# Optimization experiments

Hardware: AMD Instinct MI355X
Metric: run time of the kernel (lower is better)

Reference implementation:

```python
import jax, jax.numpy as jnp
import numpy as np

BN_EPS = 1e-5

def _bn(x, gamma, beta, relu=True):
    # training-mode BatchNorm over all dims except channel (last)
    axes = tuple(range(x.ndim - 1))
    mu = jnp.mean(x, axes, keepdims=True)
    var = jnp.var(x, axes, keepdims=True)
    y = (x - mu) / jnp.sqrt(var + BN_EPS) * gamma + beta
    return jax.nn.relu(y) if relu else y

def _l2norm(x, eps):
    # F.normalize: x / max(||x||, eps)
    n = jnp.sqrt(jnp.sum(x * x, axis=-1, keepdims=True))
    return x / jnp.maximum(n, eps)

def setup_inputs() -> dict:
    key = jax.random.key(0)
    ks = jax.random.split(key, 16)
    B, N, H, W, C = 2, 512, 16, 32, 64
    IN_DIM = 10 + C + C + 2  # 140
    MLP3 = [128, 64]
    s = 0.02
    inp = {
        "warped_xyz": jax.random.normal(ks[0], (B, N, 3), jnp.float32),
        "warped_points": jax.random.normal(ks[1], (B, N, C), jnp.float32),
        "RF3": jax.random.normal(ks[2], (B, C, H, W), jnp.float32),
        "RF3_index": jax.random.normal(ks[3], (B, 3, H, W), jnp.float32),
        "lidar_z": jax.random.uniform(ks[4], (B, N, 1), jnp.float32),
        # conv1x1 stack (mlp3)
        "W1": jax.random.normal(ks[5], (IN_DIM, MLP3[0]), jnp.float32) * s,
        "b1": jnp.zeros((MLP3[0],), jnp.float32),
        "g1": jnp.ones((MLP3[0],), jnp.float32),
        "be1": jnp.zeros((MLP3[0],), jnp.float32),
        "W2": jax.random.normal(ks[6], (MLP3[0], MLP3[1]), jnp.float32) * s,
        "b2": jnp.zeros((MLP3[1],), jnp.float32),
        "g2": jnp.ones((MLP3[1],), jnp.float32),
        "be2": jnp.zeros((MLP3[1],), jnp.float32),
        # conv1d stack (mlp4 = [feats_dim//2], then 2 logits)
        "M1w": jax.random.normal(ks[7], (MLP3[1], MLP3[1] // 2), jnp.float32) * s,
        "M1b": jnp.zeros((MLP3[1] // 2,), jnp.float32),
        "M1g": jnp.ones((MLP3[1] // 2,), jnp.float32),
        "M1be": jnp.zeros((MLP3[1] // 2,), jnp.float32),
        "M2w": jax.random.normal(ks[8], (MLP3[1] // 2, 2), jnp.float32) * s,
        "M2b": jnp.zeros((2,), jnp.float32),
    }
    return inp

def reference(warped_xyz, warped_points, RF3, RF3_index, lidar_z,
              W1, b1, g1, be1, W2, b2, g2, be2,
              M1w, M1b, M1g, M1be, M2w, M2b):
    B, N, _ = warped_xyz.shape
    _, Ci, H, W_ = RF3.shape
    M = H * W_
    RF3_bnc = RF3.transpose(0, 2, 3, 1).reshape(B, M, Ci)          # [B,M,C]
    idx_bnc = RF3_index.transpose(0, 2, 3, 1).reshape(B, M, 3)     # [B,M,3]

    src_xyz = warped_xyz[:, :, None, :]                             # [B,N,1,3]
    dst_xyz = idx_bnc[:, None, :, :]                                # [B,1,M,3]
    euc = (src_xyz - dst_xyz)[..., :2]                              # [B,N,M,2]
    euc_norm = jnp.sqrt(euc[..., 0:1] ** 2 + euc[..., 1:2] ** 2)    # [B,N,M,1]

    xyz_z = (warped_xyz * lidar_z)[:, :, None, :]                   # [B,N,1,3]
    src_pts = warped_points[:, :, None, :]                          # [B,N,1,C]
    dst_pts = RF3_bnc[:, None, :, :]                                # [B,1,M,C]

    geom = jnp.concatenate([
        jnp.broadcast_to(xyz_z, (B, N, M, 3)),
        jnp.broadcast_to(src_pts[..., :2], (B, N, M, 2)),
        jnp.broadcast_to(dst_xyz[..., :2], (B, N, M, 2)),
        euc, euc_norm], axis=-1)                                    # [B,N,M,10]
    desc = jnp.concatenate([
        jnp.broadcast_to(src_pts, (B, N, M, Ci)),
        jnp.broadcast_to(dst_pts, (B, N, M, Ci))], axis=-1)         # [B,N,M,2C]

    # cal_sim: cosine sim between lidar feats (src) and image feats (dst)
    src_n = _l2norm(warped_points, 1e-12)
    dst_n = _l2norm(RF3_bnc, 1e-12)
    cos = jnp.einsum('bnc,bmc->bnm', src_n, dst_n)                  # [B,N,M]
    s1 = cos / (jnp.max(cos, axis=2, keepdims=True) + 1e-6)         # src->dst norm
    s2 = cos / (jnp.max(cos, axis=1, keepdims=True) + 1e-10)        # dst->src norm
    sim = jnp.stack([s1, s2], axis=-1)                              # [B,N,M,2]

    feats = jnp.concatenate([geom, desc, sim], axis=-1)             # [B,N,M,140]
    feats = _bn(jnp.einsum('bnmi,io->bnmo', feats, W1) + b1, g1, be1)
    feats = _bn(jnp.einsum('bnmi,io->bnmo', feats, W2) + b2, g2, be2)

    aw = jax.nn.softmax(jnp.max(feats, axis=-1), axis=-1)           # [B,N,M]
    att = jnp.einsum('bnm,bnmc->bnc', aw, feats)                    # [B,N,C]

    att = _bn(att @ M1w + M1b, M1g, M1be)
    logits = att @ M2w + M2b                                        # [B,N,2]
    return logits
```

## Files before the change

### kernel.cpp

```cpp
#include <hip/hip_runtime.h>
#include <hip/hip_bf16.h>

#define B_ 2
#define N_ 512
#define M_ 512
#define C_ 64
#define O1 128
#define O2 64
#define O3 32
#define PBIG 524288.0f
#define P3   1024.0f

typedef short s8v __attribute__((ext_vector_type(8)));
typedef float f4v __attribute__((ext_vector_type(4)));

#define WS_SRCN 0
#define WS_DSTN 65536
#define WS_P0   0
#define WS_U    131072
#define WS_Z    131072
#define WS_V    262144
#define WS_DXY  393216
#define WS_COS  395264
#define WS_RMAX 919552
#define WS_ROWS 920576
#define WS_COLS 923648
#define WS_A1C  926720
#define WS_SC2P 935936
#define WS_ST2  936960
#define WS_ST3  945152
#define WS_CMAX 949248
#define WS_W2F  950272
#define WS_W9S  954368
#define WS_X2   961536

__device__ __forceinline__ unsigned short f2bf(float f){
  unsigned u = __float_as_uint(f);
  unsigned r = (u + 0x7fffu + ((u >> 16) & 1u)) >> 16;
  return (unsigned short)r;
}
__device__ __forceinline__ float bf2f(unsigned short h){
  return __uint_as_float(((unsigned)h) << 16);
}
__device__ __forceinline__ unsigned pk2(float lo, float hi){
  return (unsigned)f2bf(lo) | ((unsigned)f2bf(hi) << 16);
}
__device__ __forceinline__ unsigned pk_trunc(float lo, float hi){
  return __builtin_amdgcn_perm(__float_as_uint(hi), __float_as_uint(lo), 0x07060302u);
}
__device__ __forceinline__ f4v relu4(f4v z){
  z[0] = fmaxf(z[0], 0.f); z[1] = fmaxf(z[1], 0.f);
  z[2] = fmaxf(z[2], 0.f); z[3] = fmaxf(z[3], 0.f);
  return z;
}

__global__ __launch_bounds__(128) void k1(const float* __restrict__ wxyz,
    const float* __restrict__ wpts, const float* __restrict__ lz,
    const float* __restrict__ rf3, const float* __restrict__ rf3i,
    const float* __restrict__ W1, float* __restrict__ ws){
  int t = threadIdx.x;
  if (blockIdx.x < 1024){
    int blk = blockIdx.x; int b = blk >> 9, n = blk & 511;
    int bn = b*N_ + n;
    __shared__ float wp[64]; __shared__ float sxyz[3]; __shared__ float slz; __shared__ float srn;
    if (t < 64) wp[t] = wpts[bn*64 + t];
    if (t >= 64 && t < 67) sxyz[t-64] = wxyz[bn*3 + (t-64)];
    if (t == 67) slz = lz[bn];
    __syncthreads();
    if (t < 64){
      float v = wp[t]*wp[t];
      v += __shfl_down(v,32); v += __shfl_down(v,16); v += __shfl_down(v,8);
      v += __shfl_down(v,4);  v += __shfl_down(v,2);  v += __shfl_down(v,1);
      if (t == 0) srn = 1.0f / fmaxf(sqrtf(v), 1e-12f);
    }
    __syncthreads();
    if (t < 64) ws[WS_SRCN + bn*64 + t] = wp[t]*srn;
    int o = t;
    float x = sxyz[0], y = sxyz[1], z = sxyz[2], l = slz;
    float acc = x*l*W1[0*O1+o] + y*l*W1[1*O1+o] + z*l*W1[2*O1+o]
              + wp[0]*W1[3*O1+o] + wp[1]*W1[4*O1+o]
              + x*W1[7*O1+o] + y*W1[8*O1+o];
    #pragma unroll 8
    for (int c = 0; c < 64; ++c) acc += wp[c]*W1[(10+c)*O1+o];
    ws[WS_U + bn*O1 + o] = acc;
  } else {
    int blk = blockIdx.x - 1024; int b = blk >> 9, m = blk & 511;
    int bm = b*M_ + m;
    __shared__ float rf[64]; __shared__ float sdx, sdy, srn2;
    if (t < 64) rf[t] = rf3[(b*64 + t)*512 + m];
    if (t == 64) sdx = rf3i[(b*3 + 0)*512 + m];
    if (t == 65) sdy = rf3i[(b*3 + 1)*512 + m];
    __syncthreads();
    if (t < 64){
      float v = rf[t]*rf[t];
      v += __shfl_down(v,32); v += __shfl_down(v,16); v += __shfl_down(v,8);
      v += __shfl_down(v,4);  v += __shfl_down(v,2);  v += __shfl_down(v,1);
      if (t == 0) srn2 = 1.0f / fmaxf(sqrtf(v), 1e-12f);
    }
    __syncthreads();
    if (t < 64) ws[WS_DSTN + bm*64 + t] = rf[t]*srn2;
    if (t == 0){ ws[WS_DXY + bm*2+0] = sdx; ws[WS_DXY + bm*2+1] = sdy; }
    int o = t;
    float acc = sdx*(W1[5*O1+o] - W1[7*O1+o]) + sdy*(W1[6*O1+o] - W1[8*O1+o]);
    #pragma unroll 8
    for (int c = 0; c < 64; ++c) acc += rf[c]*W1[(74+c)*O1+o];
    ws[WS_V + bm*O1 + o] = acc;
  }
}

__global__ __launch_bounds__(256) void k2(float* __restrict__ ws){
  int blk = blockIdx.x; int b = blk >> 9, n = blk & 511; int t = threadIdx.x;
  int bn = b*N_ + n;
  __shared__ __align__(16) float sn[64];
  __shared__ float dnt[64*65];
  __shared__ float part[4*64];
  if (t < 64) sn[t] = ws[WS_SRCN + bn*64 + t];
  float lmax = -3.4e38f;
  for (int chunk = 0; chunk < 8; ++chunk){
    __syncthreads();
    const float4* src = (const float4*)(ws + WS_DSTN + (size_t)(b*M_ + chunk*64)*64);
    #pragma unroll
    for (int i = 0; i < 4; ++i){
      float4 v = src[t + i*256];
      int base = (t + i*256)*4; int mm = base >> 6, c = base & 63;
      float* dp = &dnt[mm*65 + c];
      dp[0]=v.x; dp[1]=v.y; dp[2]=v.z; dp[3]=v.w;
    }
    __syncthreads();
    {
      int mm = t & 63, cg = t >> 6;
      const float* dr = &dnt[mm*65 + cg*16];
      const float* sr = &sn[cg*16];
      float p = 0.f;
      #pragma unroll
      for (int k = 0; k < 16; ++k) p += sr[k]*dr[k];
      part[cg*64 + mm] = p;
    }
    __syncthreads();
    if (t < 64){
      float d = part[t] + part[64+t] + part[128+t] + part[192+t];
      ws[WS_COS + bn*M_ + chunk*64 + t] = d;
      lmax = fmaxf(lmax, d);
    }
  }
  if (t < 64){
    lmax = fmaxf(lmax, __shfl_xor(lmax,32)); lmax = fmaxf(lmax, __shfl_xor(lmax,16));
    lmax = fmaxf(lmax, __shfl_xor(lmax,8));  lmax = fmaxf(lmax, __shfl_xor(lmax,4));
    lmax = fmaxf(lmax, __shfl_xor(lmax,2));  lmax = fmaxf(lmax, __shfl_xor(lmax,1));
    if (t == 0) ws[WS_RMAX + bn] = 1.0f / (lmax + 1e-6f);
  }
}

__global__ __launch_bounds__(256) void k2r(const float* __restrict__ wxyz, float* __restrict__ ws){
  int blk = blockIdx.x;
  int b = blk >> 5; int c0 = (blk & 31)*16;
  int t = threadIdx.x;
  int cl = t & 15, seg = t >> 4;
  int col = c0 + cl;
  int bm = b*M_ + col;
  float dx = ws[WS_DXY + bm*2+0], dy = ws[WS_DXY + bm*2+1];
  float mx = -3.4e38f, se = 0.f, sc = 0.f, s1c = 0.f;
  for (int i = 0; i < 32; ++i){
    int bn = b*N_ + seg*32 + i;
    float cv = ws[WS_COS + (size_t)bn*M_ + col];
    float ri = ws[WS_RMAX + bn];
    float sx = wxyz[bn*3+0], sy = wxyz[bn*3+1];
    float ex = sx-dx, ey = sy-dy;
    se += sqrtf(ex*ex + ey*ey);
    mx = fmaxf(mx, cv);
    sc += cv;
    s1c += cv*ri;
  }
  __shared__ float r0[256], r1[256], r2[256], r3[256];
  r0[t]=mx; r1[t]=se; r2[t]=s1c; r3[t]=sc;
  __syncthreads();
  for (int s = 8; s > 0; s >>= 1){
    if (seg < s){
      int o2 = t + s*16;
      r0[t] = fmaxf(r0[t], r0[o2]); r1[t] += r1[o2]; r2[t] += r2[o2]; r3[t] += r3[o2];
    }
    __syncthreads();
  }
  if (t < 16){
    int bmw = b*M_ + c0 + t;
    float ci = 1.0f/(r0[t] + 1e-10f);
    ws[WS_CMAX + bmw] = ci;
    ws[WS_COLS + bmw] = r1[t];
    ws[WS_COLS + 1024 + bmw] = r2[t];
    ws[WS_COLS + 2048 + bmw] = r3[t]*ci;
  }
}

__global__ __launch_bounds__(256) void k3a(const float* __restrict__ wxyz, float* __restrict__ ws){
  int bn = blockIdx.x; int b = bn >> 9; int t = threadIdx.x;
  float ri = ws[WS_RMAX + bn];
  float sx = wxyz[bn*3+0], sy = wxyz[bn*3+1];
  float q[9];
  #pragma unroll
  for (int j = 0; j < 9; ++j) q[j] = 0.f;
  #pragma unroll
  for (int k = 0; k < 2; ++k){
    int m = t + k*256;
    float2 d = *(const float2*)(ws + WS_DXY + (size_t)(b*M_+m)*2);
    float ex = sx-d.x, ey = sy-d.y;
    float en = sqrtf(ex*ex + ey*ey);
    float cv = ws[WS_COS + (size_t)bn*M_ + m];
    float ci = ws[WS_CMAX + b*M_ + m];
    float s2 = cv*ci;
    q[0]+=en; q[1]+=cv; q[2]+=s2; q[3]+=en*en; q[4]+=cv*cv; q[5]+=s2*s2;
    q[6]+=en*cv; q[7]+=en*s2; q[8]+=cv*cv*ci;
  }
  #pragma unroll
  for (int j = 0; j < 9; ++j){
    float v = q[j];
    v += __shfl_xor(v,1); v += __shfl_xor(v,2); v += __shfl_xor(v,4);
    v += __shfl_xor(v,8); v += __shfl_xor(v,16); v += __shfl_xor(v,32);
    q[j] = v;
  }
  __shared__ float wr[9][4];
  int w = t >> 6;
  if ((t & 63) == 0){
    #pragma unroll
    for (int j = 0; j < 9; ++j) wr[j][w] = q[j];
  }
  __syncthreads();
  if (t < 9){
    float Q = wr[t][0] + wr[t][1] + wr[t][2] + wr[t][3];
    float f = (t==1 || t==6 || t==8) ? ri : ((t==4) ? ri*ri : 1.0f);
    float s = f*Q;
    if (t < 3) ws[WS_ROWS + t*1024 + bn] = s;
    atomicAdd(&ws[WS_SC2P + (bn & 63)*16 + t], s);
  }
}

__global__ __launch_bounds__(256) void k3s(const float* __restrict__ W1,
    const float* __restrict__ b1, const float* __restrict__ g1,
    const float* __restrict__ be1, float* __restrict__ ws){
  int o = blockIdx.x; int t = threadIdx.x;
  __shared__ float scal[9];
  __shared__ float wr[12][4];
  if (t < 9){
    float s = 0.f;
    #pragma unroll 8
    for (int r = 0; r < 64; ++r) s += ws[WS_SC2P + r*16 + t];
    scal[t] = s;
  }
  float b1o = b1[o];
  float a[12];
  #pragma unroll
  for (int j = 0; j < 12; ++j) a[j] = 0.f;
  #pragma unroll
  for (int k = 0; k < 4; ++k){
    int i = t + k*256;
    float u = ws[WS_U + (size_t)i*O1 + o] + b1o;
    float v = ws[WS_V + (size_t)i*O1 + o];
    float ren = ws[WS_ROWS + i], rs1 = ws[WS_ROWS + 1024 + i], rs2 = ws[WS_ROWS + 2048 + i];
    float cen = ws[WS_COLS + i], cs1 = ws[WS_COLS + 1024 + i], cs2 = ws[WS_COLS + 2048 + i];
    a[0]+=u; a[1]+=u*u; a[2]+=u*ren; a[3]+=u*rs1; a[4]+=u*rs2;
    a[5]+=v; a[6]+=v*v; a[7]+=v*cen; a[8]+=v*cs1; a[9]+=v*cs2;
    if (k < 2){ a[10]+=u; a[11]+=v; }
  }
  #pragma unroll
  for (int j = 0; j < 12; ++j){
    float v = a[j];
    v += __shfl_xor(v,1); v += __shfl_xor(v,2); v += __shfl_xor(v,4);
    v += __shfl_xor(v,8); v += __shfl_xor(v,16); v += __shfl_xor(v,32);
    a[j] = v;
  }
  int w = t >> 6;
  if ((t & 63) == 0){
    #pragma unroll
    for (int j = 0; j < 12; ++j) wr[j][w] = a[j];
  }
  __syncthreads();
  if (t == 0){
    float A[12];
    #pragma unroll
    for (int j = 0; j < 12; ++j) A[j] = wr[j][0] + wr[j][1] + wr[j][2] + wr[j][3];
    float w9 = W1[9*O1+o], wa = W1[138*O1+o], wb = W1[139*O1+o];
    float S1 = 512.f*(A[0] + A[5]) + w9*scal[0] + wa*scal[1] + wb*scal[2];
    float Q1 = 512.f*(A[1] + A[6])
      + 2.f*(A[10]*A[11] + (A[0]-A[10])*(A[5]-A[11]))
      + w9*w9*scal[3] + wa*wa*scal[4] + wb*wb*scal[5]
      + 2.f*(w9*wa*scal[6] + w9*wb*scal[7] + wa*wb*scal[8])
      + 2.f*(w9*A[2] + wa*A[3] + wb*A[4])
      + 2.f*(w9*A[7] + wa*A[8] + wb*A[9]);
    float mu = S1/PBIG, var = Q1/PBIG - mu*mu;
    float istd = rsqrtf(var + 1e-5f);
    float A1v = g1[o]*istd;
    ws[WS_A1C + o] = A1v;
    ws[WS_A1C + 128 + o] = be1[o] - mu*A1v;
  }
}

__global__ __launch_bounds__(128) void k3b(const float* __restrict__ W1,
    const float* __restrict__ b1, const float* __restrict__ W2, float* __restrict__ ws){
  int blk = blockIdx.x; int t = threadIdx.x; int o = t;
  float A1 = ws[WS_A1C + o], C1 = ws[WS_A1C + 128 + o];
  if (blk < 1024){
    ws[WS_P0 + blk*O1 + o] = (ws[WS_U + blk*O1 + o] + b1[o])*A1 + C1;
  } else if (blk < 1088){
    int r0 = (blk - 1024)*16;
    #pragma unroll
    for (int r = 0; r < 16; ++r)
      ws[WS_V + (size_t)(r0 + r)*O1 + o] *= A1;
  } else {
    ws[WS_W9S + o]       = W1[9*O1+o]*A1;
    ws[WS_W9S + 128 + o] = W1[138*O1+o]*A1;
    ws[WS_W9S + 256 + o] = W1[139*O1+o]*A1;
    unsigned short* wf = (unsigned short*)(ws + WS_W2F);
    for (int i = t; i < 8192; i += 128){
      int j = i & 7, ll = (i >> 3) & 63, ct = (i >> 9) & 3, k0q = i >> 11;
      int oo = k0q*32 + (ll >> 4)*8 + j, c = ct*16 + (ll & 15);
      wf[i] = f2bf(W2[oo*O2 + c]);
    }
  }
}

__global__ __launch_bounds__(256, 4) void k4(const float* __restrict__ wxyz,
    float* __restrict__ ws){
  int blk = blockIdx.x; int bn = blk >> 2, mc = blk & 3;
  int b = bn >> 9; int t = threadIdx.x;
  __shared__ __align__(16) unsigned short wBf[8192];
  __shared__ __align__(16) float p0s[128], w9s[128], was[128], wbs[128];
  __shared__ float ls[64], lq[64];
  {
    const s8v* g = (const s8v*)(ws + WS_W2F);
    s8v* l = (s8v*)wBf;
    #pragma unroll
    for (int c2 = 0; c2 < 4; ++c2) l[c2*256 + t] = g[c2*256 + t];
  }
  if (t < 64){ ls[t] = 0.f; lq[t] = 0.f; }
  if (t < 128){
    p0s[t] = ws[WS_P0 + bn*O1 + t];
    w9s[t] = ws[WS_W9S + t];
    was[t] = ws[WS_W9S + 128 + t];
    wbs[t] = ws[WS_W9S + 256 + t];
  }
  __syncthreads();
  int ll = t & 63, w = t >> 6, l16 = ll & 15, quad = ll >> 4;
  float sx = wxyz[bn*3+0], sy = wxyz[bn*3+1];
  float ri = ws[WS_RMAX + bn];
  uint4* xf4 = (uint4*)(ws + WS_X2) + (size_t)bn*4096;
  union U8 { s8v v; unsigned u[4]; };
  int mA = mc*128 + w*32 + l16, mB = mA + 16;
  float2 dA = *(const float2*)(ws + WS_DXY + (size_t)(b*M_+mA)*2);
  float2 dB = *(const float2*)(ws + WS_DXY + (size_t)(b*M_+mB)*2);
  float cvA = ws[WS_COS + (size_t)bn*M_ + mA], cvB = ws[WS_COS + (size_t)bn*M_ + mB];
  float ciA = ws[WS_CMAX + b*M_ + mA],         ciB = ws[WS_CMAX + b*M_ + mB];
  float exA = sx-dA.x, eyA = sy-dA.y; float en0 = sqrtf(exA*exA + eyA*eyA);
  float exB = sx-dB.x, eyB = sy-dB.y; float en1 = sqrtf(exB*exB + eyB*eyB);
  float s10 = cvA*ri, s20 = cvA*ciA;
  float s11 = cvB*ri, s21 = cvB*ciB;
  const float* vpA = ws + WS_V + (size_t)(b*M_+mA)*O1;
  const float* vpB = ws + WS_V + (size_t)(b*M_+mB)*O1;
  f4v acc[2][4];
  #pragma unroll
  for (int i = 0; i < 2; ++i)
    #pragma unroll
    for (int j = 0; j < 4; ++j) acc[i][j] = (f4v){0.f,0.f,0.f,0.f};
  #pragma unroll
  for (int k0q = 0; k0q < 4; ++k0q){
    int ko = k0q*32 + quad*8;
    f4v p0a = *(const f4v*)&p0s[ko], p0b = *(const f4v*)&p0s[ko+4];
    f4v w9a = *(const f4v*)&w9s[ko], w9b = *(const f4v*)&w9s[ko+4];
    f4v waa = *(const f4v*)&was[ko], wab = *(const f4v*)&was[ko+4];
    f4v wba = *(const f4v*)&wbs[ko], wbb = *(const f4v*)&wbs[ko+4];
    f4v vA0 = *(const f4v*)(vpA + ko), vA1 = *(const f4v*)(vpA + ko + 4);
    f4v vB0 = *(const f4v*)(vpB + ko), vB1 = *(const f4v*)(vpB + ko + 4);
    f4v zaA = relu4(p0a + vA0 + en0*w9a + s10*waa + s20*wba);
    f4v zbA = relu4(p0b + vA1 + en0*w9b + s10*wab + s20*wbb);
    f4v zaB = relu4(p0a + vB0 + en1*w9a + s11*waa + s21*wba);
    f4v zbB = relu4(p0b + vB1 + en1*w9b + s11*wab + s21*wbb);
    U8 uA, uB;
    uA.u[0] = pk_trunc(zaA[0], zaA[1]); uA.u[1] = pk_trunc(zaA[2], zaA[3]);
    uA.u[2] = pk_trunc(zbA[0], zbA[1]); uA.u[3] = pk_trunc(zbA[2], zbA[3]);
    uB.u[0] = pk_trunc(zaB[0], zaB[1]); uB.u[1] = pk_trunc(zaB[2], zaB[3]);
    uB.u[2] = pk_trunc(zbB[0], zbB[1]); uB.u[3] = pk_trunc(zbB[2], zbB[3]);
    #pragma unroll
    for (int ct = 0; ct < 4; ++ct){
      s8v bb = *(const s8v*)&wBf[((k0q*4 + ct)*64 + ll)*8];
      acc[0][ct] = __builtin_amdgcn_mfma_f32_16x16x32_bf16(bb, uA.v, acc[0][ct], 0,0,0);
      acc[1][ct] = __builtin_amdgcn_mfma_f32_16x16x32_bf16(bb, uB.v, acc[1][ct], 0,0,0);
    }
  }
  #pragma unroll
  for (int mt = 0; mt < 2; ++mt){
    uint4 u0, u1;
    u0.x = pk2(acc[mt][0][0], acc[mt][0][1]); u0.y = pk2(acc[mt][0][2], acc[mt][0][3]);
    u0.z = pk2(acc[mt][1][0], acc[mt][1][1]); u0.w = pk2(acc[mt][1][2], acc[mt][1][3]);
    u1.x = pk2(acc[mt][2][0], acc[mt][2][1]); u1.y = pk2(acc[mt][2][2], acc[mt][2][3]);
    u1.z = pk2(acc[mt][3][0], acc[mt][3][1]); u1.w = pk2(acc[mt][3][2], acc[mt][3][3]);
    xf4[((((mc*4 + w)*2 + mt)*2 + 0)*64) + ll] = u0;
    xf4[((((mc*4 + w)*2 + mt)*2 + 1)*64) + ll] = u1;
  }
  #pragma unroll
  for (int ct = 0; ct < 4; ++ct){
    #pragma unroll
    for (int r = 0; r < 4; ++r){
      float a0 = acc[0][ct][r], a1 = acc[1][ct][r];
      float s = a0 + a1;
      float q = a0*a0 + a1*a1;
      s += __shfl_xor(s,1); s += __shfl_xor(s,2); s += __shfl_xor(s,4); s += __shfl_xor(s,8);
      q += __shfl_xor(q,1); q += __shfl_xor(q,2); q += __shfl_xor(q,4); q += __shfl_xor(q,8);
      if (l16 == 0){
        atomicAdd(&ls[ct*16 + quad*4 + r], s);
        atomicAdd(&lq[ct*16 + quad*4 + r], q);
      }
    }
  }
  __syncthreads();
  int rep = blk & 63;
  if (t < 64) atomicAdd(&ws[WS_ST2 + rep*128 + t], ls[t]);
  else if (t < 128) atomicAdd(&ws[WS_ST2 + rep*128 + t], lq[t-64]);
}

__global__ __launch_bounds__(256) void k5(const float* __restrict__ g2,
    const float* __restrict__ be2, const float* __restrict__ M1w,
    const float* __restrict__ M1b, float* __restrict__ ws){
  int bn = blockIdx.x; int t = threadIdx.x;
  __shared__ float sa2[64], sc2[64];
  __shared__ float s_mx[512];
  __shared__ float s_aw[512];
  __shared__ float red[256];
  __shared__ float part[64*65];
  __shared__ float s_att[64];
  __shared__ float sgmax, sinvS;
  if (t < 64){
    float s = 0.f, q = 0.f;
    #pragma unroll 8
    for (int r = 0; r < 64; ++r){ s += ws[WS_ST2 + r*128 + t]; q += ws[WS_ST2 + r*128 + 64 + t]; }
    float mu = s/PBIG, var = q/PBIG - mu*mu;
    float istd = rsqrtf(var + 1e-5f);
    float A2 = g2[t]*istd;
    sa2[t] = A2; sc2[t] = be2[t] - mu*A2;
  }
  __syncthreads();
  int ll = t & 63, w = t >> 6, l16 = ll & 15, quad = ll >> 4;
  const uint4* xf4 = (const uint4*)(ws + WS_X2) + (size_t)bn*4096;
  uint4 xv[4][2][2];
  #pragma unroll
  for (int mc = 0; mc < 4; ++mc)
    #pragma unroll
    for (int mt = 0; mt < 2; ++mt)
      #pragma unroll
      for (int cp = 0; cp < 2; ++cp)
        xv[mc][mt][cp] = xf4[((((mc*4 + w)*2 + mt)*2 + cp)*64) + ll];
  float a2r[4][4], c2r[4][4];
  #pragma unroll
  for (int ct = 0; ct < 4; ++ct)
    #pragma unroll
    for (int r = 0; r < 4; ++r){
      int c = ct*16 + quad*4 + r;
      a2r[ct][r] = sa2[c]; c2r[ct][r] = sc2[c];
    }
  #pragma unroll
  for (int mc = 0; mc < 4; ++mc){
    #pragma unroll
    for (int mt = 0; mt < 2; ++mt){
      float mx = 0.f;
      #pragma unroll
      for (int cp = 0; cp < 2; ++cp){
        uint4 uv = xv[mc][mt][cp];
        int c0t = 2*cp, c1t = 2*cp + 1;
        float x0 = bf2f((unsigned short)(uv.x & 0xffffu));
        float x1 = bf2f((unsigned short)(uv.x >> 16));
        float x2 = bf2f((unsigned short)(uv.y & 0xffffu));
        float x3 = bf2f((unsigned short)(uv.y >> 16));
        float x4 = bf2f((unsigned short)(uv.z & 0xffffu));
        float x5 = bf2f((unsigned short)(uv.z >> 16));
        float x6 = bf2f((unsigned short)(uv.w & 0xffffu));
        float x7 = bf2f((unsigned short)(uv.w >> 16));
        mx = fmaxf(mx, a2r[c0t][0]*x0 + c2r[c0t][0]);
        mx = fmaxf(mx, a2r[c0t][1]*x1 + c2r[c0t][1]);
        mx = fmaxf(mx, a2r[c0t][2]*x2 + c2r[c0t][2]);
        mx = fmaxf(mx, a2r[c0t][3]*x3 + c2r[c0t][3]);
        mx = fmaxf(mx, a2r[c1t][0]*x4 + c2r[c1t][0]);
        mx = fmaxf(mx, a2r[c1t][1]*x5 + c2r[c1t][1]);
        mx = fmaxf(mx, a2r[c1t][2]*x6 + c2r[c1t][2]);
        mx = fmaxf(mx, a2r[c1t][3]*x7 + c2r[c1t][3]);
      }
      mx = fmaxf(mx, __shfl_xor(mx,16));
      mx = fmaxf(mx, __shfl_xor(mx,32));
      if (quad == 0) s_mx[mc*128 + w*32 + mt*16 + l16] = mx;
    }
  }
  __syncthreads();
  red[t] = fmaxf(s_mx[t], s_mx[t+256]);
  __syncthreads();
  for (int s = 128; s > 0; s >>= 1){ if (t < s) red[t] = fmaxf(red[t], red[t+s]); __syncthreads(); }
  if (t == 0) sgmax = red[0];
  __syncthreads();
  float e0 = expf(s_mx[t] - sgmax), e1 = expf(s_mx[t+256] - sgmax);
  s_aw[t] = e0; s_aw[t+256] = e1;
  red[t] = e0 + e1;
  __syncthreads();
  for (int s = 128; s > 0; s >>= 1){ if (t < s) red[t] += red[t+s]; __syncthreads(); }
  if (t == 0) sinvS = 1.0f / red[0];
  __syncthreads();
  float acc[4][4];
  #pragma unroll
  for (int ct = 0; ct < 4; ++ct)
    #pragma unroll
    for (int r = 0; r < 4; ++r) acc[ct][r] = 0.f;
  #pragma unroll
  for (int mc = 0; mc < 4; ++mc){
    #pragma unroll
    for (int mt = 0; mt < 2; ++mt){
      float aw = s_aw[mc*128 + w*32 + mt*16 + l16];
      #pragma unroll
      for (int cp = 0; cp < 2; ++cp){
        uint4 uv = xv[mc][mt][cp];
        int c0t = 2*cp, c1t = 2*cp + 1;
        float x0 = bf2f((unsigned short)(uv.x & 0xffffu));
        float x1 = bf2f((unsigned short)(uv.x >> 16));
        float x2 = bf2f((unsigned short)(uv.y & 0xffffu));
        float x3 = bf2f((unsigned short)(uv.y >> 16));
        float x4 = bf2f((unsigned short)(uv.z & 0xffffu));
        float x5 = bf2f((unsigned short)(uv.z >> 16));
        float x6 = bf2f((unsigned short)(uv.w & 0xffffu));
        float x7 = bf2f((unsigned short)(uv.w >> 16));
        acc[c0t][0] += aw*fmaxf(a2r[c0t][0]*x0 + c2r[c0t][0], 0.f);
        acc[c0t][1] += aw*fmaxf(a2r[c0t][1]*x1 + c2r[c0t][1], 0.f);
        acc[c0t][2] += aw*fmaxf(a2r[c0t][2]*x2 + c2r[c0t][2], 0.f);
        acc[c0t][3] += aw*fmaxf(a2r[c0t][3]*x3 + c2r[c0t][3], 0.f);
        acc[c1t][0] += aw*fmaxf(a2r[c1t][0]*x4 + c2r[c1t][0], 0.f);
        acc[c1t][1] += aw*fmaxf(a2r[c1t][1]*x5 + c2r[c1t][1], 0.f);
        acc[c1t][2] += aw*fmaxf(a2r[c1t][2]*x6 + c2r[c1t][2], 0.f);
        acc[c1t][3] += aw*fmaxf(a2r[c1t][3]*x7 + c2r[c1t][3], 0.f);
      }
    }
  }
  int row = w*16 + l16;
  #pragma unroll
  for (int ct = 0; ct < 4; ++ct)
    #pragma unroll
    for (int r = 0; r < 4; ++r)
      part[row*65 + ct*16 + quad*4 + r] = acc[ct][r];
  __syncthreads();
  if (t < 64){
    float a = 0.f;
    #pragma unroll 8
    for (int r = 0; r < 64; ++r) a += part[r*65 + t];
    s_att[t] = a * sinvS;
  }
  __syncthreads();
  if (t < 32){
    float z = M1b[t];
    #pragma unroll 8
    for (int c = 0; c < 64; ++c) z += s_att[c]*M1w[c*32 + t];
    ws[WS_Z + bn*32 + t] = z;
    int rep = bn & 63;
    atomicAdd(&ws[WS_ST3 + rep*64 + t], z);
    atomicAdd(&ws[WS_ST3 + rep*64 + 32 + t], z*z);
  }
}

__global__ __launch_bounds__(256) void k6(const float* __restrict__ M1g,
    const float* __restrict__ M1be, const float* __restrict__ M2w,
    const float* __restrict__ M2b, const float* __restrict__ ws, float* __restrict__ out){
  int t = threadIdx.x; int s = blockIdx.x*256 + t;
  __shared__ float sa3[32], sc3[32];
  if (t < 32){
    float su = 0.f, q = 0.f;
    #pragma unroll 8
    for (int r = 0; r < 64; ++r){ su += ws[WS_ST3 + r*64 + t]; q += ws[WS_ST3 + r*64 + 32 + t]; }
    float mu = su/P3, var = q/P3 - mu*mu;
    float istd = rsqrtf(var + 1e-5f);
    float A3 = M1g[t]*istd;
    sa3[t] = A3; sc3[t] = M1be[t] - mu*A3;
  }
  __syncthreads();
  float a0 = M2b[0], a1 = M2b[1];
  #pragma unroll
  for (int j = 0; j < 32; ++j){
    float y = fmaxf(ws[WS_Z + s*32 + j]*sa3[j] + sc3[j], 0.f);
    a0 += y*M2w[j*2+0]; a1 += y*M2w[j*2+1];
  }
  out[s*2+0] = a0; out[s*2+1] = a1;
}

extern "C" void kernel_launch(void* const* d_in, const int* in_sizes, int n_in,
                              void* d_out, int out_size, void* d_ws, size_t ws_size,
                              hipStream_t stream){
  const float* wxyz = (const float*)d_in[0];
  const float* wpts = (const float*)d_in[1];
  const float* rf3  = (const float*)d_in[2];
  const float* rf3i = (const float*)d_in[3];
  const float* lz   = (const float*)d_in[4];
  const float* W1   = (const float*)d_in[5];
  const float* b1   = (const float*)d_in[6];
  const float* g1   = (const float*)d_in[7];
  const float* be1  = (const float*)d_in[8];
  const float* W2   = (const float*)d_in[9];
  const float* g2   = (const float*)d_in[11];
  const float* be2  = (const float*)d_in[12];
  const float* M1w  = (const float*)d_in[13];
  const float* M1b  = (const float*)d_in[14];
  const float* M1g  = (const float*)d_in[15];
  const float* M1be = (const float*)d_in[16];
  const float* M2w  = (const float*)d_in[17];
  const float* M2b  = (const float*)d_in[18];
  float* ws  = (float*)d_ws;
  float* out = (float*)d_out;
  hipMemsetAsync(ws + WS_SC2P, 0, 13312*sizeof(float), stream);
  k1 <<<2048,128,0,stream>>>(wxyz, wpts, lz, rf3, rf3i, W1, ws);
  k2 <<<1024,256,0,stream>>>(ws);
  k2r<<<64,256,0,stream>>>(wxyz, ws);
  k3a<<<1024,256,0,stream>>>(wxyz, ws);
  k3s<<<128,256,0,stream>>>(W1, b1, g1, be1, ws);
  k3b<<<1089,128,0,stream>>>(W1, b1, W2, ws);
  k4 <<<4096,256,0,stream>>>(wxyz, ws);
  k5 <<<1024,256,0,stream>>>(g2, be2, M1w, M1b, ws);
  k6 <<<4,256,0,stream>>>(M1g, M1be, M2w, M2b, ws, out);
}
```

Measured before the change: 218.0 us.

## Fuse BN1 affine apply into stats kernel and pre-swizzle V for MFMA loads

Removes the k3b launch. The BN1 scale/shift is now applied inside k3s using the U/V values each thread already loaded, and the W2 bf16 conversion moves into an extra block of k1. The scaled V is written to a new workspace region in the exact per-lane fragment order k4 consumes, so k4's loads become contiguous per wave. The cost is scattered, uncoalesced writes in k3s (each block owns one output channel) and a larger workspace footprint.

```diff
diff --git a/kernel.cpp b/kernel.cpp
--- a/kernel.cpp
+++ b/kernel.cpp
@@ -25,7 +25,6 @@
 #define WS_RMAX 919552
 #define WS_ROWS 920576
 #define WS_COLS 923648
-#define WS_A1C  926720
 #define WS_SC2P 935936
 #define WS_ST2  936960
 #define WS_ST3  945152
@@ -33,6 +32,7 @@
 #define WS_W2F  950272
 #define WS_W9S  954368
 #define WS_X2   961536
+#define WS_VF   17738752
 
 __device__ __forceinline__ unsigned short f2bf(float f){
   unsigned u = __float_as_uint(f);
@@ -57,7 +57,7 @@
 __global__ __launch_bounds__(128) void k1(const float* __restrict__ wxyz,
     const float* __restrict__ wpts, const float* __restrict__ lz,
     const float* __restrict__ rf3, const float* __restrict__ rf3i,
-    const float* __restrict__ W1, float* __restrict__ ws){
+    const float* __restrict__ W1, const float* __restrict__ W2, float* __restrict__ ws){
   int t = threadIdx.x;
   if (blockIdx.x < 1024){
     int blk = blockIdx.x; int b = blk >> 9, n = blk & 511;
@@ -83,7 +83,7 @@
     #pragma unroll 8
     for (int c = 0; c < 64; ++c) acc += wp[c]*W1[(10+c)*O1+o];
     ws[WS_U + bn*O1 + o] = acc;
-  } else {
+  } else if (blockIdx.x < 2048){
     int blk = blockIdx.x - 1024; int b = blk >> 9, m = blk & 511;
     int bm = b*M_ + m;
     __shared__ float rf[64]; __shared__ float sdx, sdy, srn2;
@@ -105,6 +105,13 @@
     #pragma unroll 8
     for (int c = 0; c < 64; ++c) acc += rf[c]*W1[(74+c)*O1+o];
     ws[WS_V + bm*O1 + o] = acc;
+  } else {
+    unsigned short* wf = (unsigned short*)(ws + WS_W2F);
+    for (int i = t; i < 8192; i += 128){
+      int j = i & 7, ll = (i >> 3) & 63, ct = (i >> 9) & 3, k0q = i >> 11;
+      int oo = k0q*32 + (ll >> 4)*8 + j, c = ct*16 + (ll & 15);
+      wf[i] = f2bf(W2[oo*O2 + c]);
+    }
   }
 }
 
@@ -239,6 +246,7 @@
   int o = blockIdx.x; int t = threadIdx.x;
   __shared__ float scal[9];
   __shared__ float wr[12][4];
+  __shared__ float sA1, sC1;
   if (t < 9){
     float s = 0.f;
     #pragma unroll 8
@@ -246,6 +254,7 @@
     scal[t] = s;
   }
   float b1o = b1[o];
+  float uu[4], vv[4];
   float a[12];
   #pragma unroll
   for (int j = 0; j < 12; ++j) a[j] = 0.f;
@@ -254,6 +263,7 @@
     int i = t + k*256;
     float u = ws[WS_U + (size_t)i*O1 + o] + b1o;
     float v = ws[WS_V + (size_t)i*O1 + o];
+    uu[k] = u; vv[k] = v;
     float ren = ws[WS_ROWS + i], rs1 = ws[WS_ROWS + 1024 + i], rs2 = ws[WS_ROWS + 2048 + i];
     float cen = ws[WS_COLS + i], cs1 = ws[WS_COLS + 1024 + i], cs2 = ws[WS_COLS + 2048 + i];
     a[0]+=u; a[1]+=u*u; a[2]+=u*ren; a[3]+=u*rs1; a[4]+=u*rs2;
@@ -288,32 +298,22 @@
     float mu = S1/PBIG, var = Q1/PBIG - mu*mu;
     float istd = rsqrtf(var + 1e-5f);
     float A1v = g1[o]*istd;
-    ws[WS_A1C + o] = A1v;
-    ws[WS_A1C + 128 + o] = be1[o] - mu*A1v;
-  }
-}
-
-__global__ __launch_bounds__(128) void k3b(const float* __restrict__ W1,
-    const float* __restrict__ b1, const float* __restrict__ W2, float* __restrict__ ws){
-  int blk = blockIdx.x; int t = threadIdx.x; int o = t;
-  float A1 = ws[WS_A1C + o], C1 = ws[WS_A1C + 128 + o];
-  if (blk < 1024){
-    ws[WS_P0 + blk*O1 + o] = (ws[WS_U + blk*O1 + o] + b1[o])*A1 + C1;
-  } else if (blk < 1088){
-    int r0 = (blk - 1024)*16;
-    #pragma unroll
-    for (int r = 0; r < 16; ++r)
-      ws[WS_V + (size_t)(r0 + r)*O1 + o] *= A1;
-  } else {
-    ws[WS_W9S + o]       = W1[9*O1+o]*A1;
-    ws[WS_W9S + 128 + o] = W1[138*O1+o]*A1;
-    ws[WS_W9S + 256 + o] = W1[139*O1+o]*A1;
-    unsigned short* wf = (unsigned short*)(ws + WS_W2F);
-    for (int i = t; i < 8192; i += 128){
-      int j = i & 7, ll = (i >> 3) & 63, ct = (i >> 9) & 3, k0q = i >> 11;
-      int oo = k0q*32 + (ll >> 4)*8 + j, c = ct*16 + (ll & 15);
-      wf[i] = f2bf(W2[oo*O2 + c]);
-    }
+    sA1 = A1v; sC1 = be1[o] - mu*A1v;
+    ws[WS_W9S + o]       = w9*A1v;
+    ws[WS_W9S + 128 + o] = wa*A1v;
+    ws[WS_W9S + 256 + o] = wb*A1v;
+  }
+  __syncthreads();
+  float A1 = sA1, C1 = sC1;
+  int k0q = o >> 5, quad = (o >> 3) & 3, j = o & 7;
+  #pragma unroll
+  for (int k = 0; k < 4; ++k){
+    int i = t + k*256;
+    ws[WS_P0 + (size_t)i*O1 + o] = uu[k]*A1 + C1;
+    int b = i >> 9, m = i & 511;
+    int mc = m >> 7, w2 = (m >> 5) & 3, mt = (m >> 4) & 1, l16 = m & 15;
+    ws[WS_VF + (size_t)(((b*4 + mc)*4 + w2)*4096) + k0q*1024 + mt*512 + (quad*16 + l16)*8 + j]
+      = vv[k]*A1;
   }
 }
 
@@ -352,8 +352,7 @@
   float exB = sx-dB.x, eyB = sy-dB.y; float en1 = sqrtf(exB*exB + eyB*eyB);
   float s10 = cvA*ri, s20 = cvA*ciA;
   float s11 = cvB*ri, s21 = cvB*ciB;
-  const float* vpA = ws + WS_V + (size_t)(b*M_+mA)*O1;
-  const float* vpB = ws + WS_V + (size_t)(b*M_+mB)*O1;
+  const float* vfb = ws + WS_VF + (size_t)(((b*4 + mc)*4 + w)*4096) + ll*8;
   f4v acc[2][4];
   #pragma unroll
   for (int i = 0; i < 2; ++i)
@@ -366,8 +365,10 @@
     f4v w9a = *(const f4v*)&w9s[ko], w9b = *(const f4v*)&w9s[ko+4];
     f4v waa = *(const f4v*)&was[ko], wab = *(const f4v*)&was[ko+4];
     f4v wba = *(const f4v*)&wbs[ko], wbb = *(const f4v*)&wbs[ko+4];
-    f4v vA0 = *(const f4v*)(vpA + ko), vA1 = *(const f4v*)(vpA + ko + 4);
-    f4v vB0 = *(const f4v*)(vpB + ko), vB1 = *(const f4v*)(vpB + ko + 4);
+    const float* vA = vfb + k0q*1024;
+    const float* vB = vA + 512;
+    f4v vA0 = *(const f4v*)(vA), vA1 = *(const f4v*)(vA + 4);
+    f4v vB0 = *(const f4v*)(vB), vB1 = *(const f4v*)(vB + 4);
     f4v zaA = relu4(p0a + vA0 + en0*w9a + s10*waa + s20*wba);
     f4v zbA = relu4(p0b + vA1 + en0*w9b + s10*wab + s20*wbb);
     f4v zaB = relu4(p0a + vB0 + en1*w9a + s11*waa + s21*wba);
@@ -604,12 +605,11 @@
   float* ws  = (float*)d_ws;
   float* out = (float*)d_out;
   hipMemsetAsync(ws + WS_SC2P, 0, 13312*sizeof(float), stream);
-  k1 <<<2048,128,0,stream>>>(wxyz, wpts, lz, rf3, rf3i, W1, ws);
+  k1 <<<2049,128,0,stream>>>(wxyz, wpts, lz, rf3, rf3i, W1, W2, ws);
   k2 <<<1024,256,0,stream>>>(ws);
   k2r<<<64,256,0,stream>>>(wxyz, ws);
   k3a<<<1024,256,0,stream>>>(wxyz, ws);
   k3s<<<128,256,0,stream>>>(W1, b1, g1, be1, ws);
-  k3b<<<1089,128,0,stream>>>(W1, b1, W2, ws);
   k4 <<<4096,256,0,stream>>>(wxyz, ws);
   k5 <<<1024,256,0,stream>>>(g2, be2, M1w, M1b, ws);
   k6 <<<4,256,0,stream>>>(M1g, M1be, M2w, M2b, ws, out);
```

Measured after the change: 211.3 us. -3.1%, faster.
